# Optimization experiments

Hardware: AMD Instinct MI355X
Metric: run time of the kernel (lower is better)

Reference implementation:

```python
import jax, jax.numpy as jnp
import numpy as np

GROUPS = 32
EPS = 1e-5


def setup_inputs() -> dict:
    key = jax.random.key(0)
    ks = jax.random.split(key, 4)
    B, C, H, W = 32, 512, 32, 32
    x = jax.random.normal(ks[0], (B, C, H, W), dtype=jnp.float32)
    gn_gamma = jnp.ones((C,), jnp.float32)
    gn_beta = jnp.zeros((C,), jnp.float32)
    qkv_w = jax.random.normal(ks[1], (3 * C, C), dtype=jnp.float32) * 0.02
    qkv_b = jnp.zeros((3 * C,), jnp.float32)
    proj_w = jax.random.normal(ks[2], (C, C), dtype=jnp.float32) * 0.02
    proj_b = jnp.zeros((C,), jnp.float32)
    return {"x": x, "gn_gamma": gn_gamma, "gn_beta": gn_beta,
            "qkv_w": qkv_w, "qkv_b": qkv_b, "proj_w": proj_w, "proj_b": proj_b}


def group_norm(x, gamma, beta):
    B, C, H, W = x.shape
    xr = x.reshape(B, GROUPS, C // GROUPS, H, W)
    mean = xr.mean(axis=(2, 3, 4), keepdims=True)
    var = xr.var(axis=(2, 3, 4), keepdims=True)
    xn = ((xr - mean) * jax.lax.rsqrt(var + EPS)).reshape(B, C, H, W)
    return xn * gamma[None, :, None, None] + beta[None, :, None, None]


def reference(x, gn_gamma, gn_beta, qkv_w, qkv_b, proj_w, proj_b):
    B, C, H, W = x.shape
    h_in = group_norm(x, gn_gamma, gn_beta)
    # 1x1 conv == per-pixel matmul over channels
    qkv = jnp.einsum('oc,bchw->bohw', qkv_w, h_in) + qkv_b[None, :, None, None]
    q, k, v = jnp.split(qkv, 3, axis=1)
    scale = 1.0 / jnp.sqrt(jnp.sqrt(jnp.float32(C)))  # 1/sqrt(sqrt(C)), applied to q and k
    attn = jnp.einsum('bchw,bcij->bhwij', q * scale, k * scale)  # [B,H,W,H,W]
    attn = jax.nn.softmax(attn, axis=-1)  # faithful: softmax over last axis (j) only
    h = jnp.einsum('bhwij,bcij->bchw', attn, v)
    h = jnp.einsum('oc,bchw->bohw', proj_w, h) + proj_b[None, :, None, None]
    return x + h
```

## Files before the change

kernel.cpp:

```cpp
#include <hip/hip_runtime.h>

typedef __attribute__((ext_vector_type(8))) short short8;
typedef __attribute__((ext_vector_type(4))) float f32x4;

__device__ __forceinline__ float b2f(unsigned short u) {
  union { unsigned u32; float f; } x; x.u32 = ((unsigned)u) << 16; return x.f;
}
__device__ __forceinline__ unsigned short f2bf(float f) {
  union { float f; unsigned u; } x; x.f = f;
  unsigned r = x.u + 0x7fffu + ((x.u >> 16) & 1u);
  return (unsigned short)(r >> 16);
}
__device__ __forceinline__ void async_load16(const void* g, void* l) {
  __builtin_amdgcn_global_load_lds(
      (__attribute__((address_space(1))) void*)(void*)(g),
      (__attribute__((address_space(3))) void*)(l), 16, 0, 0);
}

__global__ __launch_bounds__(256) void cvt2_k(
    const float* __restrict__ a, unsigned short* __restrict__ oa, int n4a,
    const float* __restrict__ bsrc, unsigned short* __restrict__ ob, int n4b) {
  int i = blockIdx.x * 256 + threadIdx.x;
  const float* src; unsigned short* dst; int idx;
  if (i < n4a) { src = a; dst = oa; idx = i; }
  else if (i < n4a + n4b) { src = bsrc; dst = ob; idx = i - n4a; }
  else return;
  float4 v = ((const float4*)src)[idx];
  unsigned short o[4] __attribute__((aligned(8)));
  o[0] = f2bf(v.x); o[1] = f2bf(v.y); o[2] = f2bf(v.z); o[3] = f2bf(v.w);
  ((int2*)dst)[idx] = *(int2*)o;
}

__global__ __launch_bounds__(256) void groupnorm_k(
    const float* __restrict__ x, const float* __restrict__ gamma,
    const float* __restrict__ beta, unsigned short* __restrict__ hin) {
  const int b = blockIdx.x >> 5, g = blockIdx.x & 31;
  const float* xb = x + ((unsigned long long)b * 512ull + (unsigned long long)g * 16ull) * 1024ull;
  const int t = threadIdx.x;
  float4 xr[16];
  float s = 0.f, ss = 0.f;
#pragma unroll
  for (int c = 0; c < 16; ++c) {
    xr[c] = *(const float4*)(xb + c * 1024 + t * 4);
    s += xr[c].x + xr[c].y + xr[c].z + xr[c].w;
    ss += xr[c].x * xr[c].x + xr[c].y * xr[c].y + xr[c].z * xr[c].z + xr[c].w * xr[c].w;
  }
#pragma unroll
  for (int o = 32; o; o >>= 1) { s += __shfl_down(s, o); ss += __shfl_down(ss, o); }
  __shared__ float sred[8];
  if ((t & 63) == 0) { sred[t >> 6] = s; sred[4 + (t >> 6)] = ss; }
  __syncthreads();
  s = sred[0] + sred[1] + sred[2] + sred[3];
  ss = sred[4] + sred[5] + sred[6] + sred[7];
  const float mean = s * (1.f / 16384.f);
  const float rstd = rsqrtf(ss * (1.f / 16384.f) - mean * mean + 1e-5f);
  float ga[16], be[16];
#pragma unroll
  for (int c = 0; c < 16; ++c) {
    float gg = gamma[g * 16 + c] * rstd;
    ga[c] = gg;
    be[c] = beta[g * 16 + c] - mean * gg;
  }
#pragma unroll
  for (int p4 = 0; p4 < 4; ++p4) {
    unsigned short ov[16] __attribute__((aligned(16)));
#pragma unroll
    for (int c = 0; c < 16; ++c)
      ov[c] = f2bf(((const float*)&xr[c])[p4] * ga[c] + be[c]);
    unsigned short* dst = hin + ((unsigned long long)b * 1024ull + t * 4 + p4) * 512ull + g * 16;
    *(int4*)dst = *(int4*)ov;
    *(int4*)(dst + 8) = *(int4*)(ov + 8);
  }
}

template <int MODE, int MI>
__global__ __launch_bounds__(256, 2) void gemm_k(
    const unsigned short* __restrict__ A, unsigned long long sA, int lda,
    const unsigned short* __restrict__ B, unsigned long long sB, int ldb,
    const float* __restrict__ bias, const float* __restrict__ xres,
    unsigned short* __restrict__ out0, unsigned short* __restrict__ out1,
    unsigned short* __restrict__ out2, float* __restrict__ fout,
    float scale, int K) {
  constexpr int MBLK = MI * 32;
  constexpr int STAGE_SHORTS = MBLK * 64 + 128 * 64;
  constexpr int SMEM_SHORTS = (MODE == 1)
      ? ((STAGE_SHORTS > 128 * 136) ? STAGE_SHORTS : 128 * 136)
      : STAGE_SHORTS;
  __shared__ unsigned short smem[SMEM_SHORTS];
  unsigned short* As = smem;
  unsigned short* Bs = smem + MBLK * 64;
  const int tid = threadIdx.x;
  const int wave = tid >> 6, lane = tid & 63;

  int n_t, m_t, b;
  if (MODE == 0) {
    const int L = blockIdx.x + gridDim.x * (blockIdx.y + gridDim.y * blockIdx.z);
    const int r8 = L & 7, q = L >> 3;
    n_t = q % 12;
    const int mb = (q / 12) * 8 + r8;
    m_t = mb & 3;
    b = mb >> 2;
  } else if (MODE == 1) {
    const int L = blockIdx.x + gridDim.x * (blockIdx.y + gridDim.y * blockIdx.z);
    const int slice = L & 7, t = L >> 3;
    b = slice * 4 + (t >> 6);
    const int rem = t & 63;
    m_t = rem >> 3;
    n_t = rem & 7;
  } else if (MODE == 2) {
    const int L = blockIdx.x + gridDim.x * (blockIdx.y + gridDim.y * blockIdx.z);
    const int slice = L & 7, t = L >> 3;
    b = slice * 4 + (t >> 4);
    const int rem = t & 15;
    m_t = rem >> 2;
    n_t = rem & 3;
  } else {
    n_t = blockIdx.x; m_t = blockIdx.y; b = blockIdx.z;
  }
  const int m0 = m_t * MBLK, n0 = n_t * 128;
  const int wm = (wave & 1) * (MI * 16), wn = (wave >> 1) * 64;
  const unsigned short* Ab = A + (unsigned long long)b * sA + (unsigned long long)m0 * lda;
  const unsigned short* Bb = B + (unsigned long long)b * sB + (unsigned long long)n0 * ldb;

  f32x4 acc[MI][4];
#pragma unroll
  for (int i = 0; i < MI; ++i)
#pragma unroll
    for (int j = 0; j < 4; ++j)
#pragma unroll
      for (int r = 0; r < 4; ++r) acc[i][j][r] = 0.f;

  const int lrow = lane & 15;
  const int lk = lane >> 4;
  const int sr = lane >> 3;
  const int pc = (((lane & 7) ^ sr) << 3);
  const int r7 = lrow & 7;

  for (int kt = 0; kt < K; kt += 64) {
    {
#pragma unroll
      for (int c = 0; c < MBLK / 32; ++c) {
        const int row = wave * (MBLK / 4) + c * 8;
        async_load16(Ab + kt + (unsigned long long)(row + sr) * lda + pc,
                     (void*)(As + row * 64));
      }
#pragma unroll
      for (int c = 0; c < 4; ++c) {
        const int row = wave * 32 + c * 8;
        async_load16(Bb + kt + (unsigned long long)(row + sr) * ldb + pc,
                     (void*)(Bs + row * 64));
      }
    }
    __syncthreads();
#pragma unroll
    for (int ks = 0; ks < 2; ++ks) {
      const int ko = (((ks << 2) + lk) ^ r7) << 3;
      short8 af[MI], bfr[4];
#pragma unroll
      for (int i = 0; i < MI; ++i)
        af[i] = *(const short8*)(As + (wm + i * 16 + lrow) * 64 + ko);
#pragma unroll
      for (int i = 0; i < 4; ++i)
        bfr[i] = *(const short8*)(Bs + (wn + i * 16 + lrow) * 64 + ko);
#pragma unroll
      for (int mi = 0; mi < MI; ++mi)
#pragma unroll
        for (int ni = 0; ni < 4; ++ni)
          acc[mi][ni] = __builtin_amdgcn_mfma_f32_16x16x32_bf16(af[mi], bfr[ni], acc[mi][ni], 0, 0, 0);
    }
    __syncthreads();
  }

  const int r0 = lk * 4;
  const int cn = lrow;

  if (MODE == 0) {
    const int which = n0 >> 9;
#pragma unroll
    for (int ni = 0; ni < 4; ++ni) {
      const int o = n0 + wn + ni * 16 + cn;
      const float bi = bias[o];
      const int oin = o & 511;
      if (which < 2) {
        unsigned short* dst = (which == 0 ? out0 : out1) + (unsigned long long)b * 524288ull;
#pragma unroll
        for (int mi = 0; mi < MI; ++mi) {
          const int pbase = m0 + wm + mi * 16 + r0;
#pragma unroll
          for (int r = 0; r < 4; ++r)
            dst[(unsigned long long)(pbase + r) * 512ull + oin] = f2bf((acc[mi][ni][r] + bi) * scale);
        }
      } else {
        unsigned short* dst = out2 + (unsigned long long)b * 524288ull + (unsigned long long)oin * 1024ull;
#pragma unroll
        for (int mi = 0; mi < MI; ++mi) {
          const int pbase = m0 + wm + mi * 16 + r0;
          unsigned short h4[4] __attribute__((aligned(8)));
#pragma unroll
          for (int r = 0; r < 4; ++r) h4[r] = f2bf(acc[mi][ni][r] + bi);
          *(int2*)(dst + pbase) = *(int2*)h4;
        }
      }
    }
  } else if (MODE == 1) {
#pragma unroll
    for (int mi = 0; mi < MI; ++mi)
#pragma unroll
      for (int ni = 0; ni < 4; ++ni)
#pragma unroll
        for (int r = 0; r < 4; ++r) acc[mi][ni][r] = __expf(acc[mi][ni][r]);
    float inv[4][MI / 2];
#pragma unroll
    for (int ni = 0; ni < 4; ++ni)
#pragma unroll
      for (int cp = 0; cp < MI / 2; ++cp) {
        float s8 = 0.f;
#pragma unroll
        for (int mm = 0; mm < 2; ++mm)
#pragma unroll
          for (int r = 0; r < 4; ++r) s8 += acc[cp * 2 + mm][ni][r];
        s8 += __shfl_xor(s8, 16);
        s8 += __shfl_xor(s8, 32);
        inv[ni][cp] = 1.f / s8;
      }
    unsigned short* Pt = smem;
#pragma unroll
    for (int mi = 0; mi < MI; ++mi)
#pragma unroll
      for (int ni = 0; ni < 4; ++ni) {
        unsigned short p4[4] __attribute__((aligned(8)));
#pragma unroll
        for (int r = 0; r < 4; ++r) p4[r] = f2bf(acc[mi][ni][r] * inv[ni][mi >> 1]);
        const int li = wn + ni * 16 + cn;
        const int lj = wm + mi * 16 + r0;
        *(int2*)(Pt + li * 136 + lj) = *(int2*)p4;
      }
    __syncthreads();
    unsigned short* dst = out0 + (unsigned long long)b * 1048576ull;
#pragma unroll
    for (int pass = 0; pass < 8; ++pass) {
      const int row = pass * 16 + (tid >> 4);
      const int col = (tid & 15) * 8;
      int4 v = *(const int4*)(Pt + row * 136 + col);
      *(int4*)(dst + (unsigned long long)(n0 + row) * 1024ull + m0 + col) = v;
    }
  } else if (MODE == 2) {
    unsigned short* dst = out0 + (unsigned long long)b * 524288ull;
#pragma unroll
    for (int mi = 0; mi < MI; ++mi) {
      const int ib = m0 + wm + mi * 16 + r0;
#pragma unroll
      for (int ni = 0; ni < 4; ++ni) {
        const int c = n0 + wn + ni * 16 + cn;
#pragma unroll
        for (int r = 0; r < 4; ++r)
          dst[(unsigned long long)(ib + r) * 512ull + c] = f2bf(acc[mi][ni][r]);
      }
    }
  } else {
    float* dst = fout + (unsigned long long)b * 524288ull;
    const float* xr = xres + (unsigned long long)b * 524288ull;
#pragma unroll
    for (int mi = 0; mi < MI; ++mi) {
      const int ob = m0 + wm + mi * 16 + r0;
#pragma unroll
      for (int r = 0; r < 4; ++r) {
        const int o = ob + r;
        const float bi = bias[o];
#pragma unroll
        for (int ni = 0; ni < 4; ++ni) {
          const int p = n0 + wn + ni * 16 + cn;
          const unsigned long long idx = (unsigned long long)o * 1024ull + p;
          dst[idx] = acc[mi][ni][r] + bi + xr[idx];
        }
      }
    }
  }
}

extern "C" void kernel_launch(void* const* d_in, const int* in_sizes, int n_in,
                              void* d_out, int out_size, void* d_ws, size_t ws_size,
                              hipStream_t stream) {
  const float* x     = (const float*)d_in[0];
  const float* gamma = (const float*)d_in[1];
  const float* beta  = (const float*)d_in[2];
  const float* qkvw  = (const float*)d_in[3];
  const float* qkvb  = (const float*)d_in[4];
  const float* projw = (const float*)d_in[5];
  const float* projb = (const float*)d_in[6];
  float* out = (float*)d_out;
  char* ws = (char*)d_ws;

  unsigned short* Hin = (unsigned short*)(ws);
  unsigned short* Q   = (unsigned short*)(ws + 1ull * 33554432ull);
  unsigned short* Kb  = (unsigned short*)(ws + 2ull * 33554432ull);
  unsigned short* V   = (unsigned short*)(ws + 3ull * 33554432ull);
  unsigned short* S   = (unsigned short*)(ws + 4ull * 33554432ull);
  unsigned short* Wq  = (unsigned short*)(ws + 6ull * 33554432ull);
  unsigned short* Wp  = (unsigned short*)(ws + 6ull * 33554432ull + 2ull * 1048576ull);
  unsigned short* H   = Hin;

  const float SCALE = 0.21022410381342864f;
  dim3 blk(256);
  const float* nzf = nullptr;
  unsigned short* nzo = nullptr;
  float* nzfo = nullptr;

  hipLaunchKernelGGL(cvt2_k, dim3(1024), blk, 0, stream, qkvw, Wq, 196608, projw, Wp, 65536);
  hipLaunchKernelGGL(groupnorm_k, dim3(1024), blk, 0, stream, x, gamma, beta, Hin);
  hipLaunchKernelGGL((gemm_k<0, 8>), dim3(12, 4, 32), blk, 0, stream,
                     Hin, 524288ull, 512, Wq, 0ull, 512, qkvb, nzf, Q, Kb, V, nzfo, SCALE, 512);
  hipLaunchKernelGGL((gemm_k<1, 4>), dim3(8, 8, 32), blk, 0, stream,
                     Kb, 524288ull, 512, Q, 524288ull, 512, nzf, nzf, S, nzo, nzo, nzfo, 0.f, 512);
  hipLaunchKernelGGL((gemm_k<2, 8>), dim3(4, 4, 32), blk, 0, stream,
                     S, 1048576ull, 1024, V, 524288ull, 1024, nzf, nzf, H, nzo, nzo, nzfo, 0.f, 1024);
  hipLaunchKernelGGL((gemm_k<3, 8>), dim3(8, 2, 32), blk, 0, stream,
                     Wp, 0ull, 512, H, 524288ull, 512, projb, x, nzo, nzo, nzo, out, 0.f, 512);
}
```

Before: 334.9 us.

## Use 256x256 tiles with 512 threads and double-buffered LDS loads in GEMMs

Enlarges every GEMM tile to 256x256 with 8 waves per block and adds a two-stage LDS ping-pong so the next K-slice is loaded asynchronously while the current one is multiplied. This removes one barrier per K step and raises operand reuse per loaded byte. The 128 KB LDS footprint likely allows only one block per CU, reducing occupancy and latency hiding. It also shrinks grids, for example to 256 blocks for the PV GEMM, which may underfill the GPU.

```diff
diff --git a/kernel.cpp b/kernel.cpp
--- a/kernel.cpp
+++ b/kernel.cpp
@@ -73,58 +73,51 @@
   }
 }
 
-template <int MODE, int MI>
-__global__ __launch_bounds__(256, 2) void gemm_k(
+template <int MODE>
+__global__ __launch_bounds__(512, 2) void gemm_k(
     const unsigned short* __restrict__ A, unsigned long long sA, int lda,
     const unsigned short* __restrict__ B, unsigned long long sB, int ldb,
     const float* __restrict__ bias, const float* __restrict__ xres,
     unsigned short* __restrict__ out0, unsigned short* __restrict__ out1,
     unsigned short* __restrict__ out2, float* __restrict__ fout,
     float scale, int K) {
-  constexpr int MBLK = MI * 32;
-  constexpr int STAGE_SHORTS = MBLK * 64 + 128 * 64;
-  constexpr int SMEM_SHORTS = (MODE == 1)
-      ? ((STAGE_SHORTS > 128 * 136) ? STAGE_SHORTS : 128 * 136)
-      : STAGE_SHORTS;
-  __shared__ unsigned short smem[SMEM_SHORTS];
-  unsigned short* As = smem;
-  unsigned short* Bs = smem + MBLK * 64;
+  __shared__ unsigned short smem[65536];
   const int tid = threadIdx.x;
   const int wave = tid >> 6, lane = tid & 63;
 
   int n_t, m_t, b;
   if (MODE == 0) {
-    const int L = blockIdx.x + gridDim.x * (blockIdx.y + gridDim.y * blockIdx.z);
+    const int L = blockIdx.x;
     const int r8 = L & 7, q = L >> 3;
-    n_t = q % 12;
-    const int mb = (q / 12) * 8 + r8;
+    n_t = q % 6;
+    const int mb = (q / 6) * 8 + r8;
     m_t = mb & 3;
     b = mb >> 2;
   } else if (MODE == 1) {
-    const int L = blockIdx.x + gridDim.x * (blockIdx.y + gridDim.y * blockIdx.z);
-    const int slice = L & 7, t = L >> 3;
-    b = slice * 4 + (t >> 6);
-    const int rem = t & 63;
-    m_t = rem >> 3;
-    n_t = rem & 7;
-  } else if (MODE == 2) {
-    const int L = blockIdx.x + gridDim.x * (blockIdx.y + gridDim.y * blockIdx.z);
+    const int L = blockIdx.x;
     const int slice = L & 7, t = L >> 3;
     b = slice * 4 + (t >> 4);
     const int rem = t & 15;
     m_t = rem >> 2;
     n_t = rem & 3;
+  } else if (MODE == 2) {
+    const int L = blockIdx.x;
+    const int slice = L & 7, t = L >> 3;
+    b = slice * 4 + (t >> 3);
+    const int rem = t & 7;
+    m_t = rem >> 1;
+    n_t = rem & 1;
   } else {
     n_t = blockIdx.x; m_t = blockIdx.y; b = blockIdx.z;
   }
-  const int m0 = m_t * MBLK, n0 = n_t * 128;
-  const int wm = (wave & 1) * (MI * 16), wn = (wave >> 1) * 64;
+  const int m0 = m_t * 256, n0 = n_t * 256;
+  const int wm = (wave & 1) * 128, wn = (wave >> 1) * 64;
   const unsigned short* Ab = A + (unsigned long long)b * sA + (unsigned long long)m0 * lda;
   const unsigned short* Bb = B + (unsigned long long)b * sB + (unsigned long long)n0 * ldb;
 
-  f32x4 acc[MI][4];
-#pragma unroll
-  for (int i = 0; i < MI; ++i)
+  f32x4 acc[8][4];
+#pragma unroll
+  for (int i = 0; i < 8; ++i)
 #pragma unroll
     for (int j = 0; j < 4; ++j)
 #pragma unroll
@@ -135,40 +128,54 @@
   const int sr = lane >> 3;
   const int pc = (((lane & 7) ^ sr) << 3);
   const int r7 = lrow & 7;
-
-  for (int kt = 0; kt < K; kt += 64) {
-    {
-#pragma unroll
-      for (int c = 0; c < MBLK / 32; ++c) {
-        const int row = wave * (MBLK / 4) + c * 8;
-        async_load16(Ab + kt + (unsigned long long)(row + sr) * lda + pc,
-                     (void*)(As + row * 64));
-      }
+  const int arow = wave * 32;
+
+  {
+    unsigned short* As_ = smem;
+    unsigned short* Bs_ = smem + 16384;
+#pragma unroll
+    for (int c = 0; c < 4; ++c) {
+      async_load16(Ab + (unsigned long long)(arow + c * 8 + sr) * lda + pc,
+                   (void*)(As_ + (arow + c * 8) * 64));
+      async_load16(Bb + (unsigned long long)(arow + c * 8 + sr) * ldb + pc,
+                   (void*)(Bs_ + (arow + c * 8) * 64));
+    }
+  }
+  const int nt = K >> 6;
+  int cur = 0;
+  for (int t = 0; t < nt; ++t) {
+    __syncthreads();
+    if (t + 1 < nt) {
+      const int kt = (t + 1) << 6;
+      unsigned short* As_ = smem + (cur ^ 1) * 32768;
+      unsigned short* Bs_ = As_ + 16384;
 #pragma unroll
       for (int c = 0; c < 4; ++c) {
-        const int row = wave * 32 + c * 8;
-        async_load16(Bb + kt + (unsigned long long)(row + sr) * ldb + pc,
-                     (void*)(Bs + row * 64));
-      }
-    }
-    __syncthreads();
+        async_load16(Ab + kt + (unsigned long long)(arow + c * 8 + sr) * lda + pc,
+                     (void*)(As_ + (arow + c * 8) * 64));
+        async_load16(Bb + kt + (unsigned long long)(arow + c * 8 + sr) * ldb + pc,
+                     (void*)(Bs_ + (arow + c * 8) * 64));
+      }
+    }
+    const unsigned short* As = smem + cur * 32768;
+    const unsigned short* Bs = As + 16384;
 #pragma unroll
     for (int ks = 0; ks < 2; ++ks) {
       const int ko = (((ks << 2) + lk) ^ r7) << 3;
-      short8 af[MI], bfr[4];
-#pragma unroll
-      for (int i = 0; i < MI; ++i)
+      short8 af[8], bfr[4];
+#pragma unroll
+      for (int i = 0; i < 8; ++i)
         af[i] = *(const short8*)(As + (wm + i * 16 + lrow) * 64 + ko);
 #pragma unroll
       for (int i = 0; i < 4; ++i)
         bfr[i] = *(const short8*)(Bs + (wn + i * 16 + lrow) * 64 + ko);
 #pragma unroll
-      for (int mi = 0; mi < MI; ++mi)
+      for (int mi = 0; mi < 8; ++mi)
 #pragma unroll
         for (int ni = 0; ni < 4; ++ni)
           acc[mi][ni] = __builtin_amdgcn_mfma_f32_16x16x32_bf16(af[mi], bfr[ni], acc[mi][ni], 0, 0, 0);
     }
-    __syncthreads();
+    cur ^= 1;
   }
 
   const int r0 = lk * 4;
@@ -184,7 +191,7 @@
       if (which < 2) {
         unsigned short* dst = (which == 0 ? out0 : out1) + (unsigned long long)b * 524288ull;
 #pragma unroll
-        for (int mi = 0; mi < MI; ++mi) {
+        for (int mi = 0; mi < 8; ++mi) {
           const int pbase = m0 + wm + mi * 16 + r0;
 #pragma unroll
           for (int r = 0; r < 4; ++r)
@@ -193,7 +200,7 @@
       } else {
         unsigned short* dst = out2 + (unsigned long long)b * 524288ull + (unsigned long long)oin * 1024ull;
 #pragma unroll
-        for (int mi = 0; mi < MI; ++mi) {
+        for (int mi = 0; mi < 8; ++mi) {
           const int pbase = m0 + wm + mi * 16 + r0;
           unsigned short h4[4] __attribute__((aligned(8)));
 #pragma unroll
@@ -204,16 +211,16 @@
     }
   } else if (MODE == 1) {
 #pragma unroll
-    for (int mi = 0; mi < MI; ++mi)
+    for (int mi = 0; mi < 8; ++mi)
 #pragma unroll
       for (int ni = 0; ni < 4; ++ni)
 #pragma unroll
         for (int r = 0; r < 4; ++r) acc[mi][ni][r] = __expf(acc[mi][ni][r]);
-    float inv[4][MI / 2];
+    float inv[4][4];
 #pragma unroll
     for (int ni = 0; ni < 4; ++ni)
 #pragma unroll
-      for (int cp = 0; cp < MI / 2; ++cp) {
+      for (int cp = 0; cp < 4; ++cp) {
         float s8 = 0.f;
 #pragma unroll
         for (int mm = 0; mm < 2; ++mm)
@@ -224,30 +231,37 @@
         inv[ni][cp] = 1.f / s8;
       }
     unsigned short* Pt = smem;
-#pragma unroll
-    for (int mi = 0; mi < MI; ++mi)
-#pragma unroll
-      for (int ni = 0; ni < 4; ++ni) {
-        unsigned short p4[4] __attribute__((aligned(8)));
-#pragma unroll
-        for (int r = 0; r < 4; ++r) p4[r] = f2bf(acc[mi][ni][r] * inv[ni][mi >> 1]);
-        const int li = wn + ni * 16 + cn;
-        const int lj = wm + mi * 16 + r0;
-        *(int2*)(Pt + li * 136 + lj) = *(int2*)p4;
-      }
-    __syncthreads();
     unsigned short* dst = out0 + (unsigned long long)b * 1048576ull;
 #pragma unroll
-    for (int pass = 0; pass < 8; ++pass) {
-      const int row = pass * 16 + (tid >> 4);
-      const int col = (tid & 15) * 8;
-      int4 v = *(const int4*)(Pt + row * 136 + col);
-      *(int4*)(dst + (unsigned long long)(n0 + row) * 1024ull + m0 + col) = v;
+    for (int half = 0; half < 2; ++half) {
+      __syncthreads();
+      if ((wn >> 7) == half) {
+        const int lbase = wn - half * 128;
+#pragma unroll
+        for (int mi = 0; mi < 8; ++mi)
+#pragma unroll
+          for (int ni = 0; ni < 4; ++ni) {
+            unsigned short p4[4] __attribute__((aligned(8)));
+#pragma unroll
+            for (int r = 0; r < 4; ++r) p4[r] = f2bf(acc[mi][ni][r] * inv[ni][mi >> 1]);
+            const int li = lbase + ni * 16 + cn;
+            const int lj = wm + mi * 16 + r0;
+            *(int2*)(Pt + li * 264 + lj) = *(int2*)p4;
+          }
+      }
+      __syncthreads();
+#pragma unroll
+      for (int it = 0; it < 8; ++it) {
+        const int row = it * 16 + (tid >> 5);
+        const int col = (tid & 31) * 8;
+        int4 v = *(const int4*)(Pt + row * 264 + col);
+        *(int4*)(dst + (unsigned long long)(n0 + half * 128 + row) * 1024ull + m0 + col) = v;
+      }
     }
   } else if (MODE == 2) {
     unsigned short* dst = out0 + (unsigned long long)b * 524288ull;
 #pragma unroll
-    for (int mi = 0; mi < MI; ++mi) {
+    for (int mi = 0; mi < 8; ++mi) {
       const int ib = m0 + wm + mi * 16 + r0;
 #pragma unroll
       for (int ni = 0; ni < 4; ++ni) {
@@ -261,7 +275,7 @@
     float* dst = fout + (unsigned long long)b * 524288ull;
     const float* xr = xres + (unsigned long long)b * 524288ull;
 #pragma unroll
-    for (int mi = 0; mi < MI; ++mi) {
+    for (int mi = 0; mi < 8; ++mi) {
       const int ob = m0 + wm + mi * 16 + r0;
 #pragma unroll
       for (int r = 0; r < 4; ++r) {
@@ -301,19 +315,18 @@
   unsigned short* H   = Hin;
 
   const float SCALE = 0.21022410381342864f;
-  dim3 blk(256);
   const float* nzf = nullptr;
   unsigned short* nzo = nullptr;
   float* nzfo = nullptr;
 
-  hipLaunchKernelGGL(cvt2_k, dim3(1024), blk, 0, stream, qkvw, Wq, 196608, projw, Wp, 65536);
-  hipLaunchKernelGGL(groupnorm_k, dim3(1024), blk, 0, stream, x, gamma, beta, Hin);
-  hipLaunchKernelGGL((gemm_k<0, 8>), dim3(12, 4, 32), blk, 0, stream,
+  hipLaunchKernelGGL(cvt2_k, dim3(1024), dim3(256), 0, stream, qkvw, Wq, 196608, projw, Wp, 65536);
+  hipLaunchKernelGGL(groupnorm_k, dim3(1024), dim3(256), 0, stream, x, gamma, beta, Hin);
+  hipLaunchKernelGGL((gemm_k<0>), dim3(768), dim3(512), 0, stream,
                      Hin, 524288ull, 512, Wq, 0ull, 512, qkvb, nzf, Q, Kb, V, nzfo, SCALE, 512);
-  hipLaunchKernelGGL((gemm_k<1, 4>), dim3(8, 8, 32), blk, 0, stream,
+  hipLaunchKernelGGL((gemm_k<1>), dim3(512), dim3(512), 0, stream,
                      Kb, 524288ull, 512, Q, 524288ull, 512, nzf, nzf, S, nzo, nzo, nzfo, 0.f, 512);
-  hipLaunchKernelGGL((gemm_k<2, 8>), dim3(4, 4, 32), blk, 0, stream,
+  hipLaunchKernelGGL((gemm_k<2>), dim3(256), dim3(512), 0, stream,
                      S, 1048576ull, 1024, V, 524288ull, 1024, nzf, nzf, H, nzo, nzo, nzfo, 0.f, 1024);
-  hipLaunchKernelGGL((gemm_k<3, 8>), dim3(8, 2, 32), blk, 0, stream,
+  hipLaunchKernelGGL((gemm_k<3>), dim3(4, 2, 32), dim3(512), 0, stream,
                      Wp, 0ull, 512, H, 524288ull, 512, projb, x, nzo, nzo, nzo, out, 0.f, 512);
 }
```

Result: slower. 344.2 us (+2.8%).
